# Kernel optimization log

Hardware: AMD Instinct MI355X
Metric: run time of the kernel (lower is better)

The kernel has to match this reference:

```python
import jax, jax.numpy as jnp
import numpy as np

B, Q, KV, D, H = 2, 2048, 2048, 1024, 16
DH = D // H  # 64


def _rmsnorm(x, w, eps):
    return x * jax.lax.rsqrt(jnp.mean(x * x, axis=-1, keepdims=True) + eps) * w


def setup_inputs() -> dict:
    k0 = jax.random.key(0)
    ks = jax.random.split(k0, 7)
    s = 0.02
    return {
        "query": jax.random.normal(ks[0], (B, Q, D), jnp.float32),
        "key": jax.random.normal(ks[1], (B, KV, D), jnp.float32),
        "value": jax.random.normal(ks[2], (B, KV, D), jnp.float32),
        # RMSNorm weights (init to ones like nn.RMSNorm)
        "wq_norm": jnp.ones((D,), jnp.float32),
        "wk_norm": jnp.ones((D,), jnp.float32),
        # MHA in-projection for q and k (Wv / out_proj never affect attn weights)
        "Wq": jax.random.normal(ks[3], (D, D), jnp.float32) * s,
        "Wk": jax.random.normal(ks[4], (D, D), jnp.float32) * s,
        "bq": jax.random.normal(ks[5], (D,), jnp.float32) * s,
        "bk": jax.random.normal(ks[6], (D,), jnp.float32) * s,
    }


def reference(query, key, value, wq_norm, wk_norm, Wq, Wk, bq, bk):
    eps = jnp.finfo(query.dtype).eps  # nn.RMSNorm default eps
    qn = _rmsnorm(query, wq_norm, eps)
    kn = _rmsnorm(key, wk_norm, eps)
    # MHA in-projections (torch Linear: x @ W.T + b), split into heads
    q = (qn @ Wq.T + bq).reshape(B, Q, H, DH)
    k = (kn @ Wk.T + bk).reshape(B, KV, H, DH)
    # per-head scaled dot-product scores [B,H,Q,KV]
    scores = jnp.einsum('bihd,bjhd->bhij', q, k) / np.float32(np.sqrt(DH))
    # softmax over keys, then average over heads (average_attn_weights=True)
    attn = jax.nn.softmax(scores, axis=-1).mean(axis=1)  # [B,Q,KV]
    # custom re-weighting of the *separate* value tensor
    features = jnp.einsum('bij,bjd->bid', attn, value)  # [B,Q,D]
    return features
```

## Files before the change

kernel.cpp:

```cpp
#include <hip/hip_runtime.h>

#define B_  2
#define Q_  2048
#define KV_ 2048
#define D_  1024
#define H_  16
#define DH_ 64

#define QSCALE 0.18033688011112042f

using u16 = unsigned short;
using bf16x8 = __attribute__((ext_vector_type(8))) short;
using f32x4  = __attribute__((ext_vector_type(4))) float;

__device__ __forceinline__ u16 f2bf(float x) {
  unsigned u = __float_as_uint(x);
  u += 0x7fffu + ((u >> 16) & 1u);
  return (u16)(u >> 16);
}

__device__ __forceinline__ void gl_lds16(const void* g, void* l) {
  __builtin_amdgcn_global_load_lds(
      (const __attribute__((address_space(1))) void*)g,
      (__attribute__((address_space(3))) void*)l, 16, 0, 0);
}

#define MFMA16(a, b, c) __builtin_amdgcn_mfma_f32_16x16x32_bf16((a), (b), (c), 0, 0, 0)
#define EXP2F(x) __builtin_amdgcn_exp2f(x)

__global__ __launch_bounds__(256) void k_rmsnorm_cast(
    const float* __restrict__ q, const float* __restrict__ k,
    const float* __restrict__ wq, const float* __restrict__ wk,
    u16* __restrict__ qn, u16* __restrict__ kn)
{
  const int row = blockIdx.x;
  const float* src; const float* w; u16* dst;
  if (row < B_ * Q_) {
    src = q + (size_t)row * D_; w = wq; dst = qn + (size_t)row * D_;
  } else {
    const int r2 = row - B_ * Q_;
    src = k + (size_t)r2 * D_; w = wk; dst = kn + (size_t)r2 * D_;
  }
  const int t = threadIdx.x;
  float4 v = reinterpret_cast<const float4*>(src)[t];
  float ss = v.x * v.x + v.y * v.y + v.z * v.z + v.w * v.w;
  #pragma unroll
  for (int off = 1; off < 64; off <<= 1) ss += __shfl_xor(ss, off);
  __shared__ float red[4];
  if ((t & 63) == 0) red[t >> 6] = ss;
  __syncthreads();
  const float tot = red[0] + red[1] + red[2] + red[3];
  const float sc = rsqrtf(tot * (1.0f / D_) + 1.1920929e-07f);
  float4 wv = reinterpret_cast<const float4*>(w)[t];
  ushort4 o;
  o.x = f2bf(v.x * sc * wv.x);
  o.y = f2bf(v.y * sc * wv.y);
  o.z = f2bf(v.z * sc * wv.z);
  o.w = f2bf(v.w * sc * wv.w);
  reinterpret_cast<ushort4*>(dst)[t] = o;
}

__global__ __launch_bounds__(256) void k_prep_small(
    const float* __restrict__ Wq, const float* __restrict__ Wk,
    const float* __restrict__ bq, const float* __restrict__ bk,
    u16* __restrict__ Wb, float* __restrict__ biasbuf)
{
  const int bid = blockIdx.x, t = threadIdx.x;
  if (bid < 2048) {
    const int i = bid * 256 + t;
    const bool isK = i >= 262144;
    const int j = i & 262143;
    float4 v = reinterpret_cast<const float4*>(isK ? Wk : Wq)[j];
    ushort4 o;
    o.x = f2bf(v.x); o.y = f2bf(v.y); o.z = f2bf(v.z); o.w = f2bf(v.w);
    reinterpret_cast<ushort4*>(Wb + (isK ? D_ * D_ : 0))[j] = o;
  } else {
    #pragma unroll
    for (int r = 0; r < 2; ++r) {
      const int i = r * 256 + t;
      float4 v = (i < 256) ? reinterpret_cast<const float4*>(bq)[i]
                           : reinterpret_cast<const float4*>(bk)[i - 256];
      reinterpret_cast<float4*>(biasbuf)[i] = v;
    }
  }
}

__global__ __launch_bounds__(256) void k_transpose_cast_v(
    const float* __restrict__ v, u16* __restrict__ vT)
{
  const int kv0 = blockIdx.x * 64, d0 = blockIdx.y * 64, b = blockIdx.z;
  __shared__ u16 tile[64][72];
  const int t = threadIdx.x;
  #pragma unroll
  for (int i = 0; i < 16; ++i) {
    const int idx = i * 256 + t, r = idx >> 6, c = idx & 63;
    tile[r][c] = f2bf(v[((size_t)b * KV_ + kv0 + r) * D_ + d0 + c]);
  }
  __syncthreads();
  #pragma unroll
  for (int i = 0; i < 16; ++i) {
    const int idx = i * 256 + t, r = idx >> 6, c = idx & 63;
    vT[((size_t)b * D_ + d0 + r) * KV_ + kv0 + c] = tile[c][r];
  }
}

__device__ __forceinline__ int swz_off(int row, int unit) {
  return row * 64 + ((unit ^ (row & 7)) << 3);
}

template<int TM, int TN, bool OUT_BF16, bool PROJ>
__global__ __launch_bounds__(256) void k_gemm_bt(
    const u16* __restrict__ A, int lda, long sA,
    const u16* __restrict__ Bm, int ldb, long sB,
    void* __restrict__ C, int ldc, long sC,
    int K, const float* __restrict__ bias)
{
  constexpr int MR = TM / 32, NR = TN / 32;
  const int bb = blockIdx.z;
  const u16* Ab = A + (size_t)bb * sA;
  const u16* Bb = Bm + (size_t)bb * sB;
  const int row0 = blockIdx.y * TM, col0 = blockIdx.x * TN;
  __shared__ u16 As[2][TM * 64];
  __shared__ u16 Bs[2][TN * 64];
  const int tid = threadIdx.x, lane = tid & 63;
  const int w = tid >> 6, wm = w >> 1, wn = w & 1;
  const int lrow = lane & 15, sub = lane >> 4, lrow7 = lrow & 7;
  const f32x4 zero4 = {0.f, 0.f, 0.f, 0.f};
  f32x4 acc[MR][NR];
  #pragma unroll
  for (int m = 0; m < MR; ++m)
    #pragma unroll
    for (int n = 0; n < NR; ++n) acc[m][n] = zero4;

  const int nk = K >> 6;

#define GEMM_STAGE(buf, kt)                                                   \
  {                                                                           \
    const int k0 = (kt) << 6;                                                 \
    _Pragma("unroll")                                                         \
    for (int i = 0; i < TM / 32; ++i) {                                       \
      const int c = i * 256 + tid, r = c >> 3, u = (c & 7) ^ (r & 7);         \
      gl_lds16(Ab + (size_t)(row0 + r) * lda + k0 + u * 8, &As[buf][c * 8]);  \
    }                                                                         \
    _Pragma("unroll")                                                         \
    for (int i = 0; i < TN / 32; ++i) {                                       \
      const int c = i * 256 + tid, r = c >> 3, u = (c & 7) ^ (r & 7);         \
      gl_lds16(Bb + (size_t)(col0 + r) * ldb + k0 + u * 8, &Bs[buf][c * 8]);  \
    }                                                                         \
  }

  GEMM_STAGE(0, 0);
  int cur = 0;
  for (int kt = 0; kt < nk; ++kt) {
    __syncthreads();
    if (kt + 1 < nk) GEMM_STAGE(cur ^ 1, kt + 1);
    #pragma unroll
    for (int ks = 0; ks < 2; ++ks) {
      bf16x8 af[MR], bfr[NR];
      #pragma unroll
      for (int m = 0; m < MR; ++m) {
        const int rA = wm * (TM / 2) + m * 16 + lrow;
        af[m] = *(const bf16x8*)&As[cur][rA * 64 + ((((ks << 2) + sub) ^ lrow7) << 3)];
      }
      #pragma unroll
      for (int n = 0; n < NR; ++n) {
        const int rB = wn * (TN / 2) + n * 16 + lrow;
        bfr[n] = *(const bf16x8*)&Bs[cur][rB * 64 + ((((ks << 2) + sub) ^ lrow7) << 3)];
      }
      #pragma unroll
      for (int m = 0; m < MR; ++m)
        #pragma unroll
        for (int n = 0; n < NR; ++n)
          acc[m][n] = MFMA16(af[m], bfr[n], acc[m][n]);
    }
    cur ^= 1;
  }
#undef GEMM_STAGE

  const int crow = sub * 4, ccol = lane & 15;
  const float scl = (PROJ && bb == 0) ? QSCALE : 1.0f;
  #pragma unroll
  for (int m = 0; m < MR; ++m) {
    #pragma unroll
    for (int n = 0; n < NR; ++n) {
      const int gcol = col0 + wn * (TN / 2) + n * 16 + ccol;
      const float badd = PROJ ? bias[bb * 1024 + gcol] : 0.0f;
      #pragma unroll
      for (int r = 0; r < 4; ++r) {
        const int grow = row0 + wm * (TM / 2) + m * 16 + crow + r;
        const float val = (acc[m][n][r] + badd) * scl;
        if (OUT_BF16)
          ((u16*)C)[(size_t)bb * sC + (size_t)grow * ldc + gcol] = f2bf(val);
        else
          ((float*)C)[(size_t)bb * sC + (size_t)grow * ldc + gcol] = val;
      }
    }
  }
}

__global__ __launch_bounds__(256) void k_attn_rowsum(
    const u16* __restrict__ qp, const u16* __restrict__ kp,
    float* __restrict__ Linv)
{
  const int qb = blockIdx.x * 128, h = blockIdx.y, b = blockIdx.z;
  __shared__ u16 Aq[128 * 64];
  __shared__ u16 Kk[2][128 * 64];
  __shared__ float red[2][128];
  const int tid = threadIdx.x, lane = tid & 63, w = tid >> 6;
  const int wm = w >> 1, wn = w & 1;
  const int lrow = lane & 15, sub = lane >> 4, lrow7 = lrow & 7;

  #pragma unroll
  for (int i = 0; i < 4; ++i) {
    const int c = i * 256 + tid, r = c >> 3, u = (c & 7) ^ (r & 7);
    gl_lds16(&qp[((size_t)b * Q_ + qb + r) * D_ + h * 64 + u * 8], &Aq[c * 8]);
  }

#define STAGE_KK(buf, kvt)                                                    \
  {                                                                           \
    _Pragma("unroll")                                                         \
    for (int i = 0; i < 4; ++i) {                                             \
      const int c = i * 256 + tid, r = c >> 3, u = (c & 7) ^ (r & 7);         \
      gl_lds16(&kp[((size_t)b * KV_ + (kvt) * 128 + r) * D_ + h * 64 + u * 8],\
               &Kk[buf][c * 8]);                                              \
    }                                                                         \
  }

  STAGE_KK(0, 0);
  const f32x4 zero4 = {0.f, 0.f, 0.f, 0.f};
  float lsum[4][4];
  #pragma unroll
  for (int m = 0; m < 4; ++m)
    #pragma unroll
    for (int r = 0; r < 4; ++r) lsum[m][r] = 0.f;
  bf16x8 af[4][2];

  for (int kvt = 0; kvt < KV_ / 128; ++kvt) {
    const int cur = kvt & 1;
    __syncthreads();
    if (kvt == 0) {
      #pragma unroll
      for (int m = 0; m < 4; ++m) {
        const int rA = wm * 64 + m * 16 + lrow;
        af[m][0] = *(const bf16x8*)&Aq[rA * 64 + ((sub ^ lrow7) << 3)];
        af[m][1] = *(const bf16x8*)&Aq[rA * 64 + (((4 + sub) ^ lrow7) << 3)];
      }
    }
    if (kvt + 1 < KV_ / 128) STAGE_KK(cur ^ 1, kvt + 1);
    bf16x8 bf[4][2];
    #pragma unroll
    for (int n = 0; n < 4; ++n) {
      const int rB = wn * 64 + n * 16 + lrow;
      bf[n][0] = *(const bf16x8*)&Kk[cur][rB * 64 + ((sub ^ lrow7) << 3)];
      bf[n][1] = *(const bf16x8*)&Kk[cur][rB * 64 + (((4 + sub) ^ lrow7) << 3)];
    }
    #pragma unroll
    for (int m = 0; m < 4; ++m) {
      #pragma unroll
      for (int n = 0; n < 4; ++n) {
        f32x4 s = zero4;
        s = MFMA16(af[m][0], bf[n][0], s);
        s = MFMA16(af[m][1], bf[n][1], s);
        #pragma unroll
        for (int r = 0; r < 4; ++r) lsum[m][r] += EXP2F(s[r]);
      }
    }
  }
#undef STAGE_KK

  #pragma unroll
  for (int m = 0; m < 4; ++m)
    #pragma unroll
    for (int r = 0; r < 4; ++r) {
      #pragma unroll
      for (int off = 1; off < 16; off <<= 1)
        lsum[m][r] += __shfl_xor(lsum[m][r], off);
    }
  if (lrow == 0) {
    #pragma unroll
    for (int m = 0; m < 4; ++m)
      #pragma unroll
      for (int r = 0; r < 4; ++r)
        red[wn][wm * 64 + m * 16 + sub * 4 + r] = lsum[m][r];
  }
  __syncthreads();
  if (tid < 128) {
    const float s = red[0][tid] + red[1][tid];
    Linv[((size_t)b * H_ + h) * Q_ + qb + tid] = 1.0f / (s * (float)H_);
  }
}

__global__ __launch_bounds__(256, 2) void k_attn_weights(
    const u16* __restrict__ qp, const u16* __restrict__ kp,
    const float* __restrict__ Linv, u16* __restrict__ attn)
{
  const int kv0 = blockIdx.x * 128, qb = blockIdx.y * 128, b = blockIdx.z;
  __shared__ u16 As[2][128 * 64];
  __shared__ u16 Bs[2][128 * 64];
  __shared__ float linv_s[H_][128];
  const int tid = threadIdx.x, lane = tid & 63, w = tid >> 6;
  const int wm = w >> 1, wn = w & 1;
  const int lrow = lane & 15, sub = lane >> 4, lrow7 = lrow & 7;

  {
    const int hh = tid >> 4, i0 = (tid & 15) * 8;
    const float4 v0 = *reinterpret_cast<const float4*>(
        &Linv[((size_t)b * H_ + hh) * Q_ + qb + i0]);
    const float4 v1 = *reinterpret_cast<const float4*>(
        &Linv[((size_t)b * H_ + hh) * Q_ + qb + i0 + 4]);
    *reinterpret_cast<float4*>(&linv_s[hh][i0]) = v0;
    *reinterpret_cast<float4*>(&linv_s[hh][i0 + 4]) = v1;
  }

#define STAGE_AB(buf, hh)                                                     \
  {                                                                           \
    _Pragma("unroll")                                                         \
    for (int i = 0; i < 4; ++i) {                                             \
      const int c = i * 256 + tid, r = c >> 3, u = (c & 7) ^ (r & 7);         \
      gl_lds16(&qp[((size_t)b * Q_ + qb + r) * D_ + (hh) * 64 + u * 8],       \
               &As[buf][c * 8]);                                              \
      gl_lds16(&kp[((size_t)b * KV_ + kv0 + r) * D_ + (hh) * 64 + u * 8],     \
               &Bs[buf][c * 8]);                                              \
    }                                                                         \
  }

  const f32x4 zero4 = {0.f, 0.f, 0.f, 0.f};
  f32x4 acc[4][4];
  #pragma unroll
  for (int m = 0; m < 4; ++m)
    #pragma unroll
    for (int n = 0; n < 4; ++n) acc[m][n] = zero4;

  STAGE_AB(0, 0);
  for (int h = 0; h < H_; ++h) {
    const int cur = h & 1;
    __syncthreads();
    if (h + 1 < H_) STAGE_AB(cur ^ 1, h + 1);
    bf16x8 af[4][2], bf[4][2];
    #pragma unroll
    for (int m = 0; m < 4; ++m) {
      const int rA = wm * 64 + m * 16 + lrow;
      af[m][0] = *(const bf16x8*)&As[cur][rA * 64 + ((sub ^ lrow7) << 3)];
      af[m][1] = *(const bf16x8*)&As[cur][rA * 64 + (((4 + sub) ^ lrow7) << 3)];
    }
    #pragma unroll
    for (int n = 0; n < 4; ++n) {
      const int rB = wn * 64 + n * 16 + lrow;
      bf[n][0] = *(const bf16x8*)&Bs[cur][rB * 64 + ((sub ^ lrow7) << 3)];
      bf[n][1] = *(const bf16x8*)&Bs[cur][rB * 64 + (((4 + sub) ^ lrow7) << 3)];
    }
    f32x4 lv[4];
    #pragma unroll
    for (int m = 0; m < 4; ++m)
      lv[m] = *(const f32x4*)&linv_s[h][wm * 64 + m * 16 + sub * 4];
    #pragma unroll
    for (int m = 0; m < 4; ++m) {
      #pragma unroll
      for (int n = 0; n < 4; ++n) {
        f32x4 s = zero4;
        s = MFMA16(af[m][0], bf[n][0], s);
        s = MFMA16(af[m][1], bf[n][1], s);
        #pragma unroll
        for (int r = 0; r < 4; ++r)
          acc[m][n][r] += EXP2F(s[r]) * lv[m][r];
      }
    }
  }
#undef STAGE_AB

  #pragma unroll
  for (int m = 0; m < 4; ++m) {
    #pragma unroll
    for (int n = 0; n < 4; ++n) {
      const int gcol = kv0 + wn * 64 + n * 16 + lrow;
      #pragma unroll
      for (int r = 0; r < 4; ++r) {
        const int grow = qb + wm * 64 + m * 16 + sub * 4 + r;
        attn[((size_t)b * Q_ + grow) * KV_ + gcol] = f2bf(acc[m][n][r]);
      }
    }
  }
}

extern "C" void kernel_launch(void* const* d_in, const int* in_sizes, int n_in,
                              void* d_out, int out_size, void* d_ws, size_t ws_size,
                              hipStream_t stream)
{
  (void)in_sizes; (void)n_in; (void)out_size; (void)ws_size;
  const float* query = (const float*)d_in[0];
  const float* key   = (const float*)d_in[1];
  const float* value = (const float*)d_in[2];
  const float* wqn   = (const float*)d_in[3];
  const float* wkn   = (const float*)d_in[4];
  const float* Wq    = (const float*)d_in[5];
  const float* Wk    = (const float*)d_in[6];
  const float* bq    = (const float*)d_in[7];
  const float* bk    = (const float*)d_in[8];
  float* out = (float*)d_out;

  char* ws = (char*)d_ws;
  u16* qn   = (u16*)(ws);
  u16* attn = (u16*)(ws);
  u16* qp   = (u16*)(ws + 16777216);
  u16* kp   = (u16*)(ws + 25165824);
  u16* Wqb  = (u16*)(ws + 33554432);
  u16* vT   = (u16*)(ws + 37748736);
  float* Linv = (float*)(ws + 46137344);
  float* biasbuf = (float*)(ws + 46399488);
  u16* kn = qn + 4194304;

  k_rmsnorm_cast<<<dim3(B_ * Q_ + B_ * KV_), dim3(256), 0, stream>>>(
      query, key, wqn, wkn, qn, kn);
  k_prep_small<<<dim3(2049), dim3(256), 0, stream>>>(Wq, Wk, bq, bk, Wqb, biasbuf);
  k_transpose_cast_v<<<dim3(KV_ / 64, D_ / 64, B_), dim3(256), 0, stream>>>(value, vT);

  k_gemm_bt<128, 128, true, true>
      <<<dim3(D_ / 128, (B_ * Q_) / 128, 2), dim3(256), 0, stream>>>(
      qn, D_, 4194304, Wqb, D_, 1048576, qp, D_, 4194304, D_, biasbuf);

  k_attn_rowsum<<<dim3(Q_ / 128, H_, B_), dim3(256), 0, stream>>>(qp, kp, Linv);
  k_attn_weights<<<dim3(KV_ / 128, Q_ / 128, B_), dim3(256), 0, stream>>>(qp, kp, Linv, attn);

  k_gemm_bt<128, 64, false, false>
      <<<dim3(D_ / 64, Q_ / 128, B_), dim3(256), 0, stream>>>(
      attn, KV_, (long)Q_ * KV_, vT, KV_, (long)D_ * KV_,
      out, D_, (long)Q_ * D_, KV_, nullptr);
}
```

Baseline: 139.2 us.

## Merge prep kernels and overlap next-stage loads with compute via vmcnt waits

Folds the three preprocessing kernels (RMSNorm cast, weight/bias cast, V transpose) into one launch with block-range dispatch, removing two kernel launches and their inter-kernel gaps. In the GEMM and attention loops, the next tile's global-to-LDS loads are now issued before the wait, and a partial s_waitcnt vmcnt waits only for the current tile before a raw barrier, with a second barrier after compute to protect buffer reuse. This lets the prefetch run alongside the MFMA work, but it relies on hand-counted outstanding load numbers being correct, and the extra barrier per iteration adds synchronisation cost.

```diff
diff --git a/kernel.cpp b/kernel.cpp
--- a/kernel.cpp
+++ b/kernel.cpp
@@ -25,82 +25,92 @@
       (__attribute__((address_space(3))) void*)l, 16, 0, 0);
 }
 
+template<int N> __device__ __forceinline__ void wait_vmcnt() {
+  if constexpr (N == 0)      asm volatile("s_waitcnt vmcnt(0)" ::: "memory");
+  else if constexpr (N == 4) asm volatile("s_waitcnt vmcnt(4)" ::: "memory");
+  else if constexpr (N == 6) asm volatile("s_waitcnt vmcnt(6)" ::: "memory");
+  else if constexpr (N == 8) asm volatile("s_waitcnt vmcnt(8)" ::: "memory");
+}
+__device__ __forceinline__ void barrier_raw() {
+  asm volatile("" ::: "memory");
+  __builtin_amdgcn_s_barrier();
+  asm volatile("" ::: "memory");
+}
+
 #define MFMA16(a, b, c) __builtin_amdgcn_mfma_f32_16x16x32_bf16((a), (b), (c), 0, 0, 0)
 #define EXP2F(x) __builtin_amdgcn_exp2f(x)
 
-__global__ __launch_bounds__(256) void k_rmsnorm_cast(
+__global__ __launch_bounds__(256) void k_prep(
     const float* __restrict__ q, const float* __restrict__ k,
     const float* __restrict__ wq, const float* __restrict__ wk,
-    u16* __restrict__ qn, u16* __restrict__ kn)
-{
-  const int row = blockIdx.x;
-  const float* src; const float* w; u16* dst;
-  if (row < B_ * Q_) {
-    src = q + (size_t)row * D_; w = wq; dst = qn + (size_t)row * D_;
-  } else {
-    const int r2 = row - B_ * Q_;
-    src = k + (size_t)r2 * D_; w = wk; dst = kn + (size_t)r2 * D_;
-  }
-  const int t = threadIdx.x;
-  float4 v = reinterpret_cast<const float4*>(src)[t];
-  float ss = v.x * v.x + v.y * v.y + v.z * v.z + v.w * v.w;
-  #pragma unroll
-  for (int off = 1; off < 64; off <<= 1) ss += __shfl_xor(ss, off);
-  __shared__ float red[4];
-  if ((t & 63) == 0) red[t >> 6] = ss;
-  __syncthreads();
-  const float tot = red[0] + red[1] + red[2] + red[3];
-  const float sc = rsqrtf(tot * (1.0f / D_) + 1.1920929e-07f);
-  float4 wv = reinterpret_cast<const float4*>(w)[t];
-  ushort4 o;
-  o.x = f2bf(v.x * sc * wv.x);
-  o.y = f2bf(v.y * sc * wv.y);
-  o.z = f2bf(v.z * sc * wv.z);
-  o.w = f2bf(v.w * sc * wv.w);
-  reinterpret_cast<ushort4*>(dst)[t] = o;
-}
-
-__global__ __launch_bounds__(256) void k_prep_small(
     const float* __restrict__ Wq, const float* __restrict__ Wk,
     const float* __restrict__ bq, const float* __restrict__ bk,
-    u16* __restrict__ Wb, float* __restrict__ biasbuf)
+    const float* __restrict__ v,
+    u16* __restrict__ qn, u16* __restrict__ kn,
+    u16* __restrict__ Wb, float* __restrict__ biasbuf,
+    u16* __restrict__ vT)
 {
+  __shared__ char smem[64 * 72 * 2];
   const int bid = blockIdx.x, t = threadIdx.x;
-  if (bid < 2048) {
-    const int i = bid * 256 + t;
-    const bool isK = i >= 262144;
-    const int j = i & 262143;
-    float4 v = reinterpret_cast<const float4*>(isK ? Wk : Wq)[j];
+  if (bid < B_ * Q_ + B_ * KV_) {
+    const int row = bid;
+    const float* src; const float* w; u16* dst;
+    if (row < B_ * Q_) {
+      src = q + (size_t)row * D_; w = wq; dst = qn + (size_t)row * D_;
+    } else {
+      const int r2 = row - B_ * Q_;
+      src = k + (size_t)r2 * D_; w = wk; dst = kn + (size_t)r2 * D_;
+    }
+    float4 vv = reinterpret_cast<const float4*>(src)[t];
+    float ss = vv.x * vv.x + vv.y * vv.y + vv.z * vv.z + vv.w * vv.w;
+    #pragma unroll
+    for (int off = 1; off < 64; off <<= 1) ss += __shfl_xor(ss, off);
+    float* red = (float*)smem;
+    if ((t & 63) == 0) red[t >> 6] = ss;
+    __syncthreads();
+    const float tot = red[0] + red[1] + red[2] + red[3];
+    const float sc = rsqrtf(tot * (1.0f / D_) + 1.1920929e-07f);
+    float4 wv = reinterpret_cast<const float4*>(w)[t];
     ushort4 o;
-    o.x = f2bf(v.x); o.y = f2bf(v.y); o.z = f2bf(v.z); o.w = f2bf(v.w);
-    reinterpret_cast<ushort4*>(Wb + (isK ? D_ * D_ : 0))[j] = o;
+    o.x = f2bf(vv.x * sc * wv.x);
+    o.y = f2bf(vv.y * sc * wv.y);
+    o.z = f2bf(vv.z * sc * wv.z);
+    o.w = f2bf(vv.w * sc * wv.w);
+    reinterpret_cast<ushort4*>(dst)[t] = o;
+  } else if (bid < B_ * Q_ + B_ * KV_ + 2049) {
+    const int pb = bid - (B_ * Q_ + B_ * KV_);
+    if (pb < 2048) {
+      const int i = pb * 256 + t;
+      const bool isK = i >= 262144;
+      const int j = i & 262143;
+      float4 vv = reinterpret_cast<const float4*>(isK ? Wk : Wq)[j];
+      ushort4 o;
+      o.x = f2bf(vv.x); o.y = f2bf(vv.y); o.z = f2bf(vv.z); o.w = f2bf(vv.w);
+      reinterpret_cast<ushort4*>(Wb + (isK ? D_ * D_ : 0))[j] = o;
+    } else {
+      #pragma unroll
+      for (int r = 0; r < 2; ++r) {
+        const int i = r * 256 + t;
+        float4 vv = (i < 256) ? reinterpret_cast<const float4*>(bq)[i]
+                              : reinterpret_cast<const float4*>(bk)[i - 256];
+        reinterpret_cast<float4*>(biasbuf)[i] = vv;
+      }
+    }
   } else {
-    #pragma unroll
-    for (int r = 0; r < 2; ++r) {
-      const int i = r * 256 + t;
-      float4 v = (i < 256) ? reinterpret_cast<const float4*>(bq)[i]
-                           : reinterpret_cast<const float4*>(bk)[i - 256];
-      reinterpret_cast<float4*>(biasbuf)[i] = v;
-    }
-  }
-}
-
-__global__ __launch_bounds__(256) void k_transpose_cast_v(
-    const float* __restrict__ v, u16* __restrict__ vT)
-{
-  const int kv0 = blockIdx.x * 64, d0 = blockIdx.y * 64, b = blockIdx.z;
-  __shared__ u16 tile[64][72];
-  const int t = threadIdx.x;
-  #pragma unroll
-  for (int i = 0; i < 16; ++i) {
-    const int idx = i * 256 + t, r = idx >> 6, c = idx & 63;
-    tile[r][c] = f2bf(v[((size_t)b * KV_ + kv0 + r) * D_ + d0 + c]);
-  }
-  __syncthreads();
-  #pragma unroll
-  for (int i = 0; i < 16; ++i) {
-    const int idx = i * 256 + t, r = idx >> 6, c = idx & 63;
-    vT[((size_t)b * D_ + d0 + r) * KV_ + kv0 + c] = tile[c][r];
+    const int tb = bid - (B_ * Q_ + B_ * KV_ + 2049);
+    const int kv0 = (tb & 31) * 64, d0 = ((tb >> 5) & 15) * 64, b = tb >> 9;
+    u16 (*tile)[72] = (u16(*)[72])smem;
+    #pragma unroll
+    for (int i = 0; i < 16; ++i) {
+      const int idx = i * 256 + t, r = idx >> 6, c = idx & 63;
+      tile[r][c] = f2bf(v[((size_t)b * KV_ + kv0 + r) * D_ + d0 + c]);
+    }
+    __syncthreads();
+    #pragma unroll
+    for (int i = 0; i < 16; ++i) {
+      const int idx = i * 256 + t, r = idx >> 6, c = idx & 63;
+      vT[((size_t)b * D_ + d0 + r) * KV_ + kv0 + c] = tile[c][r];
+    }
   }
 }
 
@@ -116,6 +126,7 @@
     int K, const float* __restrict__ bias)
 {
   constexpr int MR = TM / 32, NR = TN / 32;
+  constexpr int NL = TM / 32 + TN / 32;
   const int bb = blockIdx.z;
   const u16* Ab = A + (size_t)bb * sA;
   const u16* Bb = Bm + (size_t)bb * sB;
@@ -152,8 +163,13 @@
   GEMM_STAGE(0, 0);
   int cur = 0;
   for (int kt = 0; kt < nk; ++kt) {
-    __syncthreads();
-    if (kt + 1 < nk) GEMM_STAGE(cur ^ 1, kt + 1);
+    if (kt + 1 < nk) {
+      GEMM_STAGE(cur ^ 1, kt + 1);
+      wait_vmcnt<NL>();
+    } else {
+      wait_vmcnt<0>();
+    }
+    barrier_raw();
     #pragma unroll
     for (int ks = 0; ks < 2; ++ks) {
       bf16x8 af[MR], bfr[NR];
@@ -173,6 +189,7 @@
         for (int n = 0; n < NR; ++n)
           acc[m][n] = MFMA16(af[m], bfr[n], acc[m][n]);
     }
+    barrier_raw();
     cur ^= 1;
   }
 #undef GEMM_STAGE
@@ -237,7 +254,13 @@
 
   for (int kvt = 0; kvt < KV_ / 128; ++kvt) {
     const int cur = kvt & 1;
-    __syncthreads();
+    if (kvt + 1 < KV_ / 128) {
+      STAGE_KK(cur ^ 1, kvt + 1);
+      wait_vmcnt<4>();
+    } else {
+      wait_vmcnt<0>();
+    }
+    barrier_raw();
     if (kvt == 0) {
       #pragma unroll
       for (int m = 0; m < 4; ++m) {
@@ -246,7 +269,6 @@
         af[m][1] = *(const bf16x8*)&Aq[rA * 64 + (((4 + sub) ^ lrow7) << 3)];
       }
     }
-    if (kvt + 1 < KV_ / 128) STAGE_KK(cur ^ 1, kvt + 1);
     bf16x8 bf[4][2];
     #pragma unroll
     for (int n = 0; n < 4; ++n) {
@@ -265,6 +287,7 @@
         for (int r = 0; r < 4; ++r) lsum[m][r] += EXP2F(s[r]);
       }
     }
+    barrier_raw();
   }
 #undef STAGE_KK
 
@@ -334,8 +357,13 @@
   STAGE_AB(0, 0);
   for (int h = 0; h < H_; ++h) {
     const int cur = h & 1;
-    __syncthreads();
-    if (h + 1 < H_) STAGE_AB(cur ^ 1, h + 1);
+    if (h + 1 < H_) {
+      STAGE_AB(cur ^ 1, h + 1);
+      wait_vmcnt<8>();
+    } else {
+      wait_vmcnt<0>();
+    }
+    barrier_raw();
     bf16x8 af[4][2], bf[4][2];
     #pragma unroll
     for (int m = 0; m < 4; ++m) {
@@ -365,6 +393,7 @@
           acc[m][n][r] += EXP2F(s[r]) * lv[m][r];
       }
     }
+    barrier_raw();
   }
 #undef STAGE_AB
 
@@ -409,10 +438,8 @@
   float* biasbuf = (float*)(ws + 46399488);
   u16* kn = qn + 4194304;
 
-  k_rmsnorm_cast<<<dim3(B_ * Q_ + B_ * KV_), dim3(256), 0, stream>>>(
-      query, key, wqn, wkn, qn, kn);
-  k_prep_small<<<dim3(2049), dim3(256), 0, stream>>>(Wq, Wk, bq, bk, Wqb, biasbuf);
-  k_transpose_cast_v<<<dim3(KV_ / 64, D_ / 64, B_), dim3(256), 0, stream>>>(value, vT);
+  k_prep<<<dim3(B_ * Q_ + B_ * KV_ + 2049 + 1024), dim3(256), 0, stream>>>(
+      query, key, wqn, wkn, Wq, Wk, bq, bk, value, qn, kn, Wqb, biasbuf, vT);
 
   k_gemm_bt<128, 128, true, true>
       <<<dim3(D_ / 128, (B_ * Q_) / 128, 2), dim3(256), 0, stream>>>(
```

Result: faster. 134.6 us (-3.3%).
